# Kernel optimization log

Hardware: AMD Instinct MI355X
Metric: run time of the kernel (lower is better)

The kernel has to match this reference:

```python
import jax, jax.numpy as jnp
import numpy as np

# einspline cubic B-spline basis matrix (4x4)
BASIS = jnp.array([[-1.0, 3.0, -3.0, 1.0],
                   [ 3.0, -6.0, 0.0, 4.0],
                   [-3.0, 3.0, 3.0, 1.0],
                   [ 1.0, 0.0, 0.0, 0.0]], dtype=jnp.float32) / 6.0


def _build_1d_system_matrix(M: int) -> jnp.ndarray:
    """(M+2, M+2) natural-boundary interpolating B-spline system matrix."""
    delta = 1.0 / (M - 1)
    dinv2 = (1.0 / delta) ** 2
    A = np.zeros((M + 2, M + 2), dtype=np.float32)
    A[0, 0] = dinv2; A[0, 1] = -2.0 * dinv2; A[0, 2] = dinv2
    i = np.arange(1, M + 1)
    A[i, i - 1] = 1.0 / 6.0
    A[i, i] = 2.0 / 3.0
    A[i, i + 1] = 1.0 / 6.0
    A[M + 1, M - 1] = dinv2; A[M + 1, M] = -2.0 * dinv2; A[M + 1, M + 1] = dinv2
    return jnp.asarray(A)


def find_coefs_2d(data: jnp.ndarray) -> jnp.ndarray:
    """data: (C, Mx, My) -> coefs: (C, Mx+2, My+2) via separable solves."""
    C, Mx, My = data.shape
    Ax = _build_1d_system_matrix(Mx)
    Ay = _build_1d_system_matrix(My)
    # solve along x for every (c, y)
    d = jnp.transpose(data, (0, 2, 1)).reshape(-1, Mx)          # (C*My, Mx)
    Bx = jnp.zeros((d.shape[0], Mx + 2), dtype=data.dtype).at[:, 1:Mx + 1].set(d)
    cx = jnp.linalg.solve(Ax, Bx.T).T                           # (C*My, Mx+2)
    cx = jnp.transpose(cx.reshape(C, My, Mx + 2), (0, 2, 1))    # (C, Mx+2, My)
    # solve along y for every (c, x)
    d2 = cx.reshape(-1, My)                                      # (C*(Mx+2), My)
    By = jnp.zeros((d2.shape[0], My + 2), dtype=data.dtype).at[:, 1:My + 1].set(d2)
    coefs = jnp.linalg.solve(Ay, By.T).T.reshape(C, Mx + 2, My + 2)
    return coefs


def _axis_index(un: jnp.ndarray, M: int):
    """Cell index + local fraction with out-of-range extrapolation handling."""
    i = jnp.floor(un).astype(jnp.int32)
    t = un - i.astype(un.dtype)
    low = un < 0
    i = jnp.where(low, 0, i)
    t = jnp.where(low, un, t)
    high = un >= M - 2
    i = jnp.where(high, M - 2, i)
    t = jnp.where(high, un - (M - 2), t)
    return i, t


def interpolate_grid_2d(coefs: jnp.ndarray, u: jnp.ndarray) -> jnp.ndarray:
    """coefs: (C, Mx+2, My+2); u: (B, 2) in [0,1]^2 -> (B, C)."""
    C, Mxp2, Myp2 = coefs.shape
    Mx, My = Mxp2 - 2, Myp2 - 2
    ux_norm = u[:, 0] * (Mx - 1)
    uy_norm = u[:, 1] * (My - 1)
    ix, tx = _axis_index(ux_norm, Mx)
    iy, ty = _axis_index(uy_norm, My)
    ones = jnp.ones_like(tx)
    tx_powers = jnp.stack([tx ** 3, tx ** 2, tx, ones], axis=0)  # (4, B)
    ty_powers = jnp.stack([ty ** 3, ty ** 2, ty, ones], axis=0)  # (4, B)
    basis_x = BASIS @ tx_powers                                   # (4, B)
    basis_y = BASIS @ ty_powers                                   # (4, B)
    offsets = jnp.arange(4, dtype=jnp.int32)
    ix_exp = ix[None, :] + offsets[:, None]                       # (4, B)
    iy_exp = iy[None, :] + offsets[:, None]                       # (4, B)
    # 4x4 neighborhood gather: (C, 4, 4, B)
    control_grid = coefs[:, ix_exp[:, None, :], iy_exp[None, :, :]]
    intermediate = jnp.einsum('cijb,ib->cjb', control_grid, basis_x)
    values = jnp.einsum('cjb,jb->cb', intermediate, basis_y)
    return values.T                                               # (B, C)


def setup_inputs() -> dict:
    key = jax.random.key(0)
    k_u, k_d = jax.random.split(key)
    u = jax.random.uniform(k_u, (2000000, 2), dtype=jnp.float32)
    data = jax.random.normal(k_d, (4, 64, 64), dtype=jnp.float32)
    return {"u": u, "data": data}


def reference(u, data):
    coefs = find_coefs_2d(data)
    return interpolate_grid_2d(coefs, u)
```

## Files before the change

### kernel.cpp

```cpp
#include <hip/hip_runtime.h>
#include <math.h>

#define MX 64
#define NC 4
#define NI 66
#define NINT 62

typedef _Float16 half4  __attribute__((ext_vector_type(4)));
typedef _Float16 half2v __attribute__((ext_vector_type(2)));

struct TC { float m[NINT]; float inv[NINT]; };
constexpr TC make_tc() {
    TC tc{};
    double dp = 2.0/3.0;
    tc.m[0] = 0.0f;
    tc.inv[0] = (float)(1.0/dp);
    for (int j = 1; j < NINT; ++j) {
        double m = (1.0/6.0) / dp;
        tc.m[j] = (float)m;
        dp = 2.0/3.0 - m*(1.0/6.0);
        tc.inv[j] = (float)(1.0/dp);
    }
    return tc;
}
__constant__ constexpr TC g_tc = make_tc();

__device__ __forceinline__ float4 eval_pt(const half4* __restrict__ lds,
                                          float ux, float uy)
{
    const float unx = ux * 63.0f;
    const float uny = uy * 63.0f;

    int ix = (int)unx; ix = ix > 62 ? 62 : ix;
    int iy = (int)uny; iy = iy > 62 ? 62 : iy;
    const float tx = unx - (float)ix;
    const float ty = uny - (float)iy;

    const half2v t = __builtin_bit_cast(half2v, __builtin_amdgcn_cvt_pkrtz(tx, ty));
    const half2v c16  = half2v{(_Float16)(1.0f/6.0f), (_Float16)(1.0f/6.0f)};
    const half2v ch   = half2v{(_Float16)0.5f,  (_Float16)0.5f};
    const half2v cnh  = half2v{(_Float16)-0.5f, (_Float16)-0.5f};
    const half2v cn16 = half2v{(_Float16)(-1.0f/6.0f), (_Float16)(-1.0f/6.0f)};
    const half2v cn1  = half2v{(_Float16)-1.0f, (_Float16)-1.0f};
    const half2v c23  = half2v{(_Float16)(2.0f/3.0f), (_Float16)(2.0f/3.0f)};

    const half2v t2 = t*t;
    half2v b0 = (cn16*t + ch)*t;  b0 = (b0 + cnh)*t + c16;
    half2v b1 = (ch*t + cn1)*t2 + c23;
    half2v b2 = (cnh*t + ch)*t;   b2 = (b2 + ch)*t + c16;
    half2v b3 = c16*(t*t2);

    const half2v by0 = __builtin_shufflevector(b0, b0, 1, 1);
    const half2v by1 = __builtin_shufflevector(b1, b1, 1, 1);
    const half2v by2 = __builtin_shufflevector(b2, b2, 1, 1);
    const half2v by3 = __builtin_shufflevector(b3, b3, 1, 1);
    const half2v bx[4] = {
        __builtin_shufflevector(b0, b0, 0, 0),
        __builtin_shufflevector(b1, b1, 0, 0),
        __builtin_shufflevector(b2, b2, 0, 0),
        __builtin_shufflevector(b3, b3, 0, 0),
    };

    const half4* r = lds + (ix*NI + iy);
    half2v t01, t23;
    #pragma unroll
    for (int ar = 0; ar < 4; ++ar) {
        const half4 c0 = r[ar*NI + 0];
        const half4 c1 = r[ar*NI + 1];
        const half4 c2 = r[ar*NI + 2];
        const half4 c3 = r[ar*NI + 3];
        half2v a01 = c0.lo*by0 + c1.lo*by1 + c2.lo*by2 + c3.lo*by3;
        half2v a23 = c0.hi*by0 + c1.hi*by1 + c2.hi*by2 + c3.hi*by3;
        if (ar == 0) { t01 = a01*bx[0];        t23 = a23*bx[0]; }
        else         { t01 = a01*bx[ar] + t01; t23 = a23*bx[ar] + t23; }
    }
    return make_float4((float)t01.x, (float)t01.y, (float)t23.x, (float)t23.y);
}

__global__ __launch_bounds__(512, 4) void fused(const float4* __restrict__ u2,
                                                const float*  __restrict__ data,
                                                float4* __restrict__ out, int NB)
{
    __shared__ half4 chS[NI*NI];
    __shared__ float cxS[2][NI][65];
    const int t = threadIdx.x;
    const float a = 1.0f/6.0f;

    #pragma unroll
    for (int c2 = 0; c2 < 2; ++c2) {
        if (t < 128) {
            const int cl = t >> 6, y = t & 63;
            const int c  = c2*2 + cl;
            const float* g = data + c*(MX*MX) + y;
            float w[NINT];
            const float d0 = g[0];
            #pragma unroll
            for (int j = 0; j < NINT; ++j) w[j] = g[(j+1)*MX];
            const float dM = g[63*MX];
            w[0]      -= a*d0;
            w[NINT-1] -= a*dM;
            #pragma unroll
            for (int j = 1; j < NINT; ++j) w[j] -= g_tc.m[j]*w[j-1];
            float x = w[NINT-1] * g_tc.inv[NINT-1];
            const float c63 = x;
            cxS[cl][63][y] = x;
            #pragma unroll
            for (int j = NINT-2; j >= 0; --j) {
                x = (w[j] - a*x) * g_tc.inv[j];
                cxS[cl][j+2][y] = x;
            }
            cxS[cl][0][y]  = 2.0f*d0 - x;
            cxS[cl][1][y]  = d0;
            cxS[cl][64][y] = dM;
            cxS[cl][65][y] = 2.0f*dM - c63;
        }
        __syncthreads();

        if (t < 2*NI) {
            const int cl = t / NI;
            const int i  = t - cl*NI;
            const int c  = c2*2 + cl;
            const float* g = &cxS[cl][i][0];
            _Float16* o = ((_Float16*)&chS[i*NI]) + c;

            float w[NINT];
            const float d0 = g[0];
            #pragma unroll
            for (int j = 0; j < NINT; ++j) w[j] = g[j+1];
            const float dM = g[63];
            w[0]      -= a*d0;
            w[NINT-1] -= a*dM;
            #pragma unroll
            for (int j = 1; j < NINT; ++j) w[j] -= g_tc.m[j]*w[j-1];
            float x = w[NINT-1] * g_tc.inv[NINT-1];
            const float c63 = x;
            o[63*NC] = (_Float16)x;
            #pragma unroll
            for (int j = NINT-2; j >= 0; --j) {
                x = (w[j] - a*x) * g_tc.inv[j];
                o[(j+2)*NC] = (_Float16)x;
            }
            o[0*NC]  = (_Float16)(2.0f*d0 - x);
            o[1*NC]  = (_Float16)d0;
            o[64*NC] = (_Float16)dM;
            o[65*NC] = (_Float16)(2.0f*dM - c63);
        }
        __syncthreads();
    }

    const int stride = gridDim.x * 512;
    for (int b = blockIdx.x*512 + t; b < NB; b += stride) {
        const float4 uu = u2[b];
        const float4 v0 = eval_pt(chS, uu.x, uu.y);
        const float4 v1 = eval_pt(chS, uu.z, uu.w);
        out[2*b]   = v0;
        out[2*b+1] = v1;
    }
}

extern "C" void kernel_launch(void* const* d_in, const int* in_sizes, int n_in,
                              void* d_out, int out_size, void* d_ws, size_t ws_size,
                              hipStream_t stream)
{
    const float* u    = (const float*)d_in[0];
    const float* data = (const float*)d_in[1];
    const int B  = in_sizes[0] / 2;
    const int NB = B / 2;

    fused<<<512, 512, 0, stream>>>((const float4*)u, data, (float4*)d_out, NB);
}
```

Before: 87.12 us.

## Duplicate coefficient table into even/odd-aligned copies for 16-byte LDS loads

Builds a second shifted copy of the fp16 coefficient table in the reused scratch arena so that each 4-wide row of the stencil can be fetched with two aligned 16-byte LDS reads instead of four 8-byte reads, selecting the even or odd copy by the parity of iy. The evaluation loop also switches from two points per thread to one point per thread with float2 input loads. This adds a copy pass and a barrier per block and may change occupancy and memory coalescing of the point loop.

```diff
diff --git a/kernel.cpp b/kernel.cpp
--- a/kernel.cpp
+++ b/kernel.cpp
@@ -7,6 +7,7 @@
 #define NINT 62
 
 typedef _Float16 half4  __attribute__((ext_vector_type(4)));
+typedef _Float16 half8  __attribute__((ext_vector_type(8)));
 typedef _Float16 half2v __attribute__((ext_vector_type(2)));
 
 struct TC { float m[NINT]; float inv[NINT]; };
@@ -25,7 +26,8 @@
 }
 __constant__ constexpr TC g_tc = make_tc();
 
-__device__ __forceinline__ float4 eval_pt(const half4* __restrict__ lds,
+__device__ __forceinline__ float4 eval_pt(const char* __restrict__ taB,
+                                          const char* __restrict__ tbB,
                                           float ux, float uy)
 {
     const float unx = ux * 63.0f;
@@ -61,28 +63,41 @@
         __builtin_shufflevector(b3, b3, 0, 0),
     };
 
-    const half4* r = lds + (ix*NI + iy);
+    const int odd = iy & 1;
+    const int ke  = iy >> 1;
+    const char* base    = odd ? tbB : taB;
+    const int   rstride = odd ? 512 : 528;
+    const char* rp = base + ix*rstride + ke*16;
+
     half2v t01, t23;
     #pragma unroll
     for (int ar = 0; ar < 4; ++ar) {
-        const half4 c0 = r[ar*NI + 0];
-        const half4 c1 = r[ar*NI + 1];
-        const half4 c2 = r[ar*NI + 2];
-        const half4 c3 = r[ar*NI + 3];
-        half2v a01 = c0.lo*by0 + c1.lo*by1 + c2.lo*by2 + c3.lo*by3;
-        half2v a23 = c0.hi*by0 + c1.hi*by1 + c2.hi*by2 + c3.hi*by3;
+        const half8 p0 = *(const half8*)(rp);
+        const half8 p1 = *(const half8*)(rp + 16);
+        rp += rstride;
+        const half2v e0c01 = __builtin_shufflevector(p0, p0, 0, 1);
+        const half2v e0c23 = __builtin_shufflevector(p0, p0, 2, 3);
+        const half2v e1c01 = __builtin_shufflevector(p0, p0, 4, 5);
+        const half2v e1c23 = __builtin_shufflevector(p0, p0, 6, 7);
+        const half2v e2c01 = __builtin_shufflevector(p1, p1, 0, 1);
+        const half2v e2c23 = __builtin_shufflevector(p1, p1, 2, 3);
+        const half2v e3c01 = __builtin_shufflevector(p1, p1, 4, 5);
+        const half2v e3c23 = __builtin_shufflevector(p1, p1, 6, 7);
+        half2v a01 = e0c01*by0 + e1c01*by1 + e2c01*by2 + e3c01*by3;
+        half2v a23 = e0c23*by0 + e1c23*by1 + e2c23*by2 + e3c23*by3;
         if (ar == 0) { t01 = a01*bx[0];        t23 = a23*bx[0]; }
         else         { t01 = a01*bx[ar] + t01; t23 = a23*bx[ar] + t23; }
     }
     return make_float4((float)t01.x, (float)t01.y, (float)t23.x, (float)t23.y);
 }
 
-__global__ __launch_bounds__(512, 4) void fused(const float4* __restrict__ u2,
+__global__ __launch_bounds__(512, 4) void fused(const float2* __restrict__ uv,
                                                 const float*  __restrict__ data,
-                                                float4* __restrict__ out, int NB)
+                                                float4* __restrict__ out, int B)
 {
-    __shared__ half4 chS[NI*NI];
-    __shared__ float cxS[2][NI][65];
+    __shared__ __align__(16) half4 chS[NI*NI];
+    __shared__ __align__(16) char  arenaB[2*NI*65*4];
+    float (*cxS)[NI][65] = (float(*)[NI][65])arenaB;
     const int t = threadIdx.x;
     const float a = 1.0f/6.0f;
 
@@ -148,13 +163,23 @@
         __syncthreads();
     }
 
+    {
+        half4* TB4 = (half4*)arenaB;
+        for (int s = t; s < NI*32; s += 512) {
+            const int i = s >> 5, k = s & 31;
+            const half4* src = chS + i*NI + 2*k + 1;
+            TB4[(i*32 + k)*2 + 0] = src[0];
+            TB4[(i*32 + k)*2 + 1] = src[1];
+        }
+    }
+    __syncthreads();
+
+    const char* taB = (const char*)chS;
+    const char* tbB = (const char*)arenaB;
     const int stride = gridDim.x * 512;
-    for (int b = blockIdx.x*512 + t; b < NB; b += stride) {
-        const float4 uu = u2[b];
-        const float4 v0 = eval_pt(chS, uu.x, uu.y);
-        const float4 v1 = eval_pt(chS, uu.z, uu.w);
-        out[2*b]   = v0;
-        out[2*b+1] = v1;
+    for (int b = blockIdx.x*512 + t; b < B; b += stride) {
+        const float2 uu = uv[b];
+        out[b] = eval_pt(taB, tbB, uu.x, uu.y);
     }
 }
 
@@ -165,7 +190,6 @@
     const float* u    = (const float*)d_in[0];
     const float* data = (const float*)d_in[1];
     const int B  = in_sizes[0] / 2;
-    const int NB = B / 2;
 
-    fused<<<512, 512, 0, stream>>>((const float4*)u, data, (float4*)d_out, NB);
+    fused<<<512, 512, 0, stream>>>((const float2*)u, data, (float4*)d_out, B);
 }
```

Measured after the change: 82.96 us. 4.8% less time.
